# Kernel optimization log

Measured on AMD Instinct MI355X. Metric: run time of the kernel, lower is better.

The kernel has to match this reference:

```python
import jax, jax.numpy as jnp
import numpy as np
from jax.scipy.linalg import cholesky, solve_triangular, cho_solve

N, M, D = 16384, 2048, 8
VAR, LS = 1.0, 0.5      # RBF kernel hyperparameters (same for kernel_f and kernel_g)
JITTER = 1e-6
BATCH_RATE = 1.0
HALF_LOG_2PI = 0.5 * float(np.log(2.0 * np.pi))


def rbf(x1, x2):
    # K[i,j] = VAR * exp(-||x1_i - x2_j||^2 / (2 LS^2))
    d2 = (jnp.sum(x1 * x1, 1)[:, None] + jnp.sum(x2 * x2, 1)[None, :]
          - 2.0 * (x1 @ x2.T))
    return VAR * jnp.exp(-0.5 * d2 / (LS * LS))


def setup_inputs() -> dict:
    key = jax.random.key(0)
    ks = jax.random.split(key, 7)
    x = jax.random.normal(ks[0], (N, D), dtype=jnp.float32)
    y = jax.random.normal(ks[1], (N, 1), dtype=jnp.float32)
    z = 2.0 * jax.random.uniform(ks[2], (M, D), dtype=jnp.float32) - 1.0  # inducing inputs in [-1,1]^D
    q_m_f = 0.5 * jax.random.normal(ks[3], (M, 1), dtype=jnp.float32)
    q_m_g = 0.5 * jax.random.normal(ks[4], (M, 1), dtype=jnp.float32)
    # Cholesky-like params: identity plus small strictly-lower noise -> PD covariance
    q_L_f = jnp.eye(M, dtype=jnp.float32) + 0.01 * jnp.tril(
        jax.random.normal(ks[5], (M, M), dtype=jnp.float32), -1)
    q_L_g = jnp.eye(M, dtype=jnp.float32) + 0.01 * jnp.tril(
        jax.random.normal(ks[6], (M, M), dtype=jnp.float32), -1)
    return {"x": x, "y": y, "z": z, "q_m_f": q_m_f, "q_L_f": q_L_f,
            "q_m_g": q_m_g, "q_L_g": q_L_g}


def _gp_marginals_and_kl(x, z, q_m, q_L_raw):
    """Marginal posterior mean/var at x and KL(q(u)||p(u)) for one sparse GP."""
    L_S = jnp.tril(q_L_raw)                     # [M,M]
    Kuu = rbf(z, z) + JITTER * jnp.eye(M, dtype=x.dtype)
    Lk = cholesky(Kuu, lower=True)
    Kfu = rbf(x, z)                             # [N,M]
    # A = Kfu @ Kuu^{-1}
    A = cho_solve((Lk, True), Kfu.T).T          # [N,M]
    m = (A @ q_m)[:, 0]                         # [N]
    # diag(Kff + A (S - Kuu) A^T) = diag(Kff) + diag(A S A^T) - diag(Kfu A^T)
    S = L_S @ L_S.T
    diag_Kff = jnp.full((x.shape[0],), VAR, dtype=x.dtype)
    v = diag_Kff + jnp.sum((A @ S) * A, axis=1) - jnp.sum(A * Kfu, axis=1)
    # KL(N(q_m, S) || N(0, Kuu))
    alpha = solve_triangular(Lk, q_m, lower=True)       # Kuu^{-1/2} m
    W = solve_triangular(Lk, L_S, lower=True)           # Kuu^{-1/2} L_S
    logdet_K = 2.0 * jnp.sum(jnp.log(jnp.diag(Lk)))
    logdet_S = 2.0 * jnp.sum(jnp.log(jnp.abs(jnp.diag(L_S))))
    kl = 0.5 * (jnp.sum(W * W) + jnp.sum(alpha * alpha)
                - jnp.asarray(M, x.dtype) + logdet_K - logdet_S)
    return m, v, kl


def reference(x, y, z, q_m_f, q_L_f, q_m_g, q_L_g):
    m_f, v_f, kl_f = _gp_marginals_and_kl(x, z, q_m_f, q_L_f)
    m_g, v_g, kl_g = _gp_marginals_and_kl(x, z, q_m_g, q_L_g)
    yv = y[:, 0]
    # HetGaussian variational expectation (Saul et al. 2016):
    # E_q[log N(y | f, exp(g))] per point
    expectation = (-HALF_LOG_2PI - 0.5 * m_g
                   - 0.5 * ((yv - m_f) ** 2 + v_f) * jnp.exp(-m_g + 0.5 * v_g))
    elbo = BATCH_RATE * jnp.sum(expectation) - (kl_f + kl_g)
    return -elbo
```

## Files before the change

kernel.cpp:

```cpp
#include <hip/hip_runtime.h>
#include <math.h>

#define NN 16384
#define MM 2048
#define DD 8
#define NB 32
#define SZB ((size_t)16777216)

constexpr float HLOG2PI = 0.91893853320467274178f;

using short8  = __attribute__((ext_vector_type(8))) short;
using float4v = __attribute__((ext_vector_type(4))) float;

__device__ __forceinline__ float4v f4zero(){ float4v v; v[0]=0.f; v[1]=0.f; v[2]=0.f; v[3]=0.f; return v; }

__device__ __forceinline__ void bfsplit(float v, short& h, short& lo){
  unsigned b = __float_as_uint(v);
  h = (short)(b >> 16);
  float hf = __uint_as_float(b & 0xFFFF0000u);
  lo = (short)(__float_as_uint(v - hf) >> 16);
}
__device__ __forceinline__ float bf2f(short s){
  return __uint_as_float(((unsigned)(unsigned short)s) << 16);
}
__device__ __forceinline__ float4v mfma3(short8 ah, short8 al, short8 bh, short8 bl, float4v c){
  c = __builtin_amdgcn_mfma_f32_16x16x32_bf16(ah, bh, c, 0, 0, 0);
  c = __builtin_amdgcn_mfma_f32_16x16x32_bf16(ah, bl, c, 0, 0, 0);
  c = __builtin_amdgcn_mfma_f32_16x16x32_bf16(al, bh, c, 0, 0, 0);
  return c;
}

__device__ __forceinline__ float block_reduce(float v, float* scratch){
  int lane = threadIdx.x & 63;
  int w    = threadIdx.x >> 6;
  #pragma unroll
  for (int off=32; off; off>>=1) v += __shfl_down(v, off, 64);
  __syncthreads();
  if (lane==0) scratch[w] = v;
  __syncthreads();
  float r = 0.f;
  if (threadIdx.x < 4) r = scratch[threadIdx.x];
  if (w==0){ r += __shfl_down(r, 2, 64); r += __shfl_down(r, 1, 64); }
  return r;
}

__device__ __forceinline__ void stage64(float (*S)[68], const float* __restrict__ g, int ld, int t){
  #pragma unroll
  for (int p=t; p<1024; p+=256)
    *(float4*)&S[p>>4][(p&15)*4] = *(const float4*)&g[(size_t)(p>>4)*ld + (p&15)*4];
}
__device__ __forceinline__ void tile_gemm_step(float acc[4][4], const float (*As)[68], const float (*Bs)[68], int tx, int ty){
  for (int k=0;k<64;++k){
    float ar[4], bc4[4];
    #pragma unroll
    for (int u=0;u<4;++u){ ar[u]=As[ty*4+u][k]; bc4[u]=Bs[k][tx*4+u]; }
    #pragma unroll
    for (int u=0;u<4;++u)
      #pragma unroll
      for (int v=0;v<4;++v) acc[u][v] += ar[u]*bc4[v];
  }
}
__device__ __forceinline__ void tile_syrk_step(float acc[4][4], const float (*P)[68], const float (*Q)[68], int tx, int ty){
  for (int k=0;k<64;++k){
    float pr[4], qc[4];
    #pragma unroll
    for (int u=0;u<4;++u){ pr[u]=P[ty*4+u][k]; qc[u]=Q[tx*4+u][k]; }
    #pragma unroll
    for (int u=0;u<4;++u)
      #pragma unroll
      for (int v=0;v<4;++v) acc[u][v] += pr[u]*qc[v];
  }
}

__device__ __forceinline__ void factor64_reg(const float (*S)[68],
    float* __restrict__ lkd, float* __restrict__ sdg_, int d, int t){
  if (t < 64){
    float xr[64];
    #pragma unroll
    for (int c4=0;c4<16;++c4) *(float4*)&xr[c4*4] = *(const float4*)&S[t][c4*4];
    float myrp = 1.f;
    #pragma unroll
    for (int j=0;j<64;++j){
      float ajj = __shfl(xr[j], j, 64);
      float piv = sqrtf(fmaxf(ajj, 1e-20f));
      float rp  = 1.f/piv;
      float val = xr[j]*rp;
      if (t==j){ xr[j] = piv; myrp = rp; }
      else if (t>j) xr[j] = val;
      else val = 0.f;
      #pragma unroll
      for (int c=j+1;c<64;++c){
        float vc = __shfl(val, c, 64);
        if (c<=t) xr[c] -= val*vc;
      }
    }
    #pragma unroll
    for (int c=0;c<64;++c) if (c>t) xr[c] = 0.f;
    #pragma unroll
    for (int c4=0;c4<16;++c4)
      *(float4*)&lkd[d*4096 + t*64 + c4*4] = *(float4*)&xr[c4*4];
    sdg_[d*64 + t] = myrp;
  }
}


__global__ __launch_bounds__(256) void phase0_kernel(
    const float* __restrict__ z, float* __restrict__ kuu){
  __shared__ float As[64][68];
  __shared__ float Bs[64][68];
  const int t = threadIdx.x, tx = t & 15, ty = t >> 4;
  int idx = blockIdx.x;
  int r=0; while ((r+1)*(r+2)/2 <= idx) ++r;
  int c = idx - r*(r+1)/2;
  for (int p=t; p<128; p+=256){ int i=p>>1, h=p&1;
    *(float4*)&As[i][h*4] = *(const float4*)&z[(size_t)(r*64+i)*DD + h*4];
    *(float4*)&Bs[i][h*4] = *(const float4*)&z[(size_t)(c*64+i)*DD + h*4]; }
  __syncthreads();
  #pragma unroll
  for (int u=0;u<4;++u){
    float4 o;
    float* ov = (float*)&o;
    #pragma unroll
    for (int v=0;v<4;++v){
      float d2=0.f;
      #pragma unroll
      for (int d=0;d<8;++d){ float df=As[ty*4+u][d]-Bs[tx*4+v][d]; d2+=df*df; }
      float val = __expf(-2.f*d2);
      if (r*64+ty*4+u == c*64+tx*4+v) val += 1e-6f;
      ov[v] = val;
    }
    *(float4*)&kuu[(size_t)(r*64+ty*4+u)*MM + c*64 + tx*4] = o;
  }
}

__global__ __launch_bounds__(256) void diag0_kernel(
    const float* __restrict__ kuu, float* __restrict__ lkdiag, float* __restrict__ sdg){
  __shared__ float As[64][68];
  const int t = threadIdx.x;
  stage64(As, kuu, MM, t);
  __syncthreads();
  factor64_reg(As, lkdiag, sdg, 0, t);
}

__global__ __launch_bounds__(256) void panel_kernel(
    float* __restrict__ kuu, float* __restrict__ lkdiag,
    float* __restrict__ sdg, float* __restrict__ ltri, int kb){
  __shared__ float As[64][68];
  __shared__ float Bs[64][68];
  __shared__ float Cs[64][68];
  __shared__ float sd[64];
  const int t = threadIdx.x, tx = t & 15, ty = t >> 4;
  int idx = blockIdx.x;
  int r=0; while ((r+1)*(r+2)/2 <= idx) ++r;
  int c = idx - r*(r+1)/2;
  int bi = kb+1+r, bc = kb+1+c;
  stage64(Cs, lkdiag + kb*4096, 64, t);
  if (t < 64) sd[t] = sdg[kb*64 + t];
  stage64(As, kuu + (size_t)(bi*64)*MM + kb*64, MM, t);
  if (bc != bi) stage64(Bs, kuu + (size_t)(bc*64)*MM + kb*64, MM, t);
  __syncthreads();
  {
    int w = t>>6, l = t&63;
    if (w==0 || (w==1 && bc!=bi)){
      float (*S)[68] = (w==0)? As : Bs;
      float xr[64];
      #pragma unroll
      for (int c4=0;c4<16;++c4) *(float4*)&xr[c4*4] = *(const float4*)&S[l][c4*4];
      #pragma unroll
      for (int j=0;j<64;++j){
        float xj = xr[j]*sd[j];
        xr[j] = xj;
        #pragma unroll
        for (int cc=j+1;cc<64;++cc) xr[cc] -= xj*Cs[cc][j];
      }
      #pragma unroll
      for (int c4=0;c4<16;++c4) *(float4*)&S[l][c4*4] = *(float4*)&xr[c4*4];
    }
  }
  __syncthreads();
  if (bc == kb+1){
    for (int p=t;p<1024;p+=256)
      *(float4*)&ltri[(size_t)(bi*64+(p>>4))*MM + kb*64 + (p&15)*4] =
          *(float4*)&As[p>>4][(p&15)*4];
  }
  float acc[4][4] = {};
  tile_syrk_step(acc, As, (bc==bi)? As : Bs, tx, ty);
  if (bi==kb+1 && bc==kb+1){
    __syncthreads();
    #pragma unroll
    for (int u=0;u<4;++u)
      #pragma unroll
      for (int v=0;v<4;++v) Bs[ty*4+u][tx*4+v] = acc[u][v];
    __syncthreads();
    for (int p=t;p<1024;p+=256){
      int i=p>>4, c4=p&15;
      float4 kv = *(const float4*)&kuu[(size_t)(bi*64+i)*MM + bi*64 + c4*4];
      float4 bv = *(float4*)&Bs[i][c4*4];
      float4 o; o.x=kv.x-bv.x; o.y=kv.y-bv.y; o.z=kv.z-bv.z; o.w=kv.w-bv.w;
      *(float4*)&As[i][c4*4] = o;
    }
    __syncthreads();
    factor64_reg(As, lkdiag, sdg, kb+1, t);
  } else {
    #pragma unroll
    for (int u=0;u<4;++u){
      float4* dst = (float4*)&kuu[(size_t)(bi*64+ty*4+u)*MM + bc*64 + tx*4];
      float4 o = *dst;
      o.x-=acc[u][0]; o.y-=acc[u][1]; o.z-=acc[u][2]; o.w-=acc[u][3];
      *dst = o;
    }
  }
}

__global__ __launch_bounds__(256) void phase2_kernel(
    const float* __restrict__ lkdiag, float* __restrict__ linv){
  __shared__ float As[64][68];
  __shared__ float Bs[64][68];
  const int t = threadIdx.x, bid = blockIdx.x;
  stage64(As, lkdiag + bid*4096, 64, t);
  __syncthreads();
  if (t < 64){
    for (int j=0;j<64;++j){
      float s = (j==t)?1.f:0.f;
      for (int k=t;k<j;++k) s -= As[j][k]*Bs[k][t];
      Bs[j][t] = (j>=t)? s/As[j][j] : 0.f;
    }
  }
  __syncthreads();
  for (int p=t;p<1024;p+=256){ int i=p>>4, c4=p&15;
    *(float4*)&linv[(size_t)(bid*64+i)*MM + bid*64 + c4*4] = *(float4*)&Bs[i][c4*4]; }
}

__global__ __launch_bounds__(256) void p3l0_kernel(
    const float* __restrict__ ltri, float* __restrict__ linv){
  __shared__ float As[64][68];
  __shared__ float Bs[64][68];
  const int t = threadIdx.x, tx = t & 15, ty = t >> 4;
  int m = blockIdx.x;
  stage64(As, ltri + (size_t)((2*m+1)*64)*MM + (2*m)*64, MM, t);
  stage64(Bs, linv + (size_t)((2*m)*64)*MM   + (2*m)*64, MM, t);
  __syncthreads();
  float acc[4][4]={};
  tile_gemm_step(acc, As, Bs, tx, ty);
  __syncthreads();
  #pragma unroll
  for (int u=0;u<4;++u)
    #pragma unroll
    for (int v=0;v<4;++v) Bs[ty*4+u][tx*4+v] = acc[u][v];
  stage64(As, linv + (size_t)((2*m+1)*64)*MM + (2*m+1)*64, MM, t);
  __syncthreads();
  float o[4][4]={};
  tile_gemm_step(o, As, Bs, tx, ty);
  #pragma unroll
  for (int u=0;u<4;++u)
    *(float4*)&linv[(size_t)((2*m+1)*64+ty*4+u)*MM + (2*m)*64 + tx*4] =
        make_float4(-o[u][0],-o[u][1],-o[u][2],-o[u][3]);
}

__global__ __launch_bounds__(256) void p3l1_kernel(
    const float* __restrict__ ltri, float* __restrict__ linv, float* __restrict__ ptmp){
  __shared__ float As[64][68];
  __shared__ float Bs[64][68];
  const int t = threadIdx.x, tx = t & 15, ty = t >> 4;
  int m = blockIdx.x;
  float* pm = ptmp + (size_t)m*128*128;
  for (int ti=0; ti<2; ++ti)
    for (int tj=0; tj<2; ++tj){
      int rb = m*4 + 2 + ti, cb0 = m*4;
      float acc[4][4]={};
      for (int k=tj; k<2; ++k){
        __syncthreads();
        stage64(As, ltri + (size_t)(rb*64)*MM + (cb0+k)*64, MM, t);
        stage64(Bs, linv + (size_t)((cb0+k)*64)*MM + (cb0+tj)*64, MM, t);
        __syncthreads();
        tile_gemm_step(acc, As, Bs, tx, ty);
      }
      #pragma unroll
      for (int u=0;u<4;++u)
        *(float4*)&pm[(size_t)(ti*64+ty*4+u)*128 + tj*64 + tx*4] =
            make_float4(acc[u][0],acc[u][1],acc[u][2],acc[u][3]);
    }
  for (int ti=0; ti<2; ++ti)
    for (int tj=0; tj<2; ++tj){
      int rb = m*4 + 2 + ti;
      float acc[4][4]={};
      for (int k=0; k<=ti; ++k){
        __syncthreads();
        stage64(As, linv + (size_t)(rb*64)*MM + (m*4+2+k)*64, MM, t);
        stage64(Bs, pm + (size_t)(k*64)*128 + tj*64, 128, t);
        __syncthreads();
        tile_gemm_step(acc, As, Bs, tx, ty);
      }
      #pragma unroll
      for (int u=0;u<4;++u)
        *(float4*)&linv[(size_t)(rb*64+ty*4+u)*MM + (m*4+tj)*64 + tx*4] =
            make_float4(-acc[u][0],-acc[u][1],-acc[u][2],-acc[u][3]);
    }
}

__global__ __launch_bounds__(256) void p3lA_kernel(
    const float* __restrict__ ltri, const float* __restrict__ linv,
    float* __restrict__ ptmp, int s){
  __shared__ float As[64][68];
  __shared__ float Bs[64][68];
  const int t = threadIdx.x, tx = t & 15, ty = t >> 4;
  int nb = 1<<s, b = 64<<s;
  float* pmb = ptmp + (s==2 ? 131072 : (s==3 ? 393216 : 917504));
  int idx = blockIdx.x;
  int m = idx/(nb*nb), r2 = idx%(nb*nb);
  int ti = r2/nb, tj = r2%nb;
  int rb = m*2*nb + nb + ti, cb0 = m*2*nb;
  float acc[4][4]={};
  for (int k=tj; k<nb; ++k){
    __syncthreads();
    stage64(As, ltri + (size_t)(rb*64)*MM + (cb0+k)*64, MM, t);
    stage64(Bs, linv + (size_t)((cb0+k)*64)*MM + (cb0+tj)*64, MM, t);
    __syncthreads();
// ... 29 lines not shown
  #pragma unroll
  for (int u=0;u<4;++u)
    *(float4*)&linv[(size_t)(rb*64+ty*4+u)*MM + (m*2*nb+tj)*64 + tx*4] =
        make_float4(-acc[u][0],-acc[u][1],-acc[u][2],-acc[u][3]);
}

__global__ __launch_bounds__(256) void w_kernel(
    const float* __restrict__ linv, const float* __restrict__ qlf,
    const float* __restrict__ qlg, float* __restrict__ wf, float* __restrict__ wg){
  __shared__ float As[64][68];
  __shared__ float Bs[64][68];
  const int t = threadIdx.x, tx = t & 15, ty = t >> 4;
  int idx = blockIdx.x;
  int gp = idx/528, rem = idx%528;
  int bi=0; while ((bi+1)*(bi+2)/2 <= rem) ++bi;
  int bj = rem - bi*(bi+1)/2;
  const float* ql = gp ? qlg : qlf;
  float* w        = gp ? wg  : wf;
  float acc[4][4]={};
  for (int bk=bj; bk<=bi; ++bk){
    __syncthreads();
    stage64(As, linv + (size_t)(bi*64)*MM + bk*64, MM, t);
    stage64(Bs, ql   + (size_t)(bk*64)*MM + bj*64, MM, t);
    __syncthreads();
    if (bk==bj){
      for (int p=t;p<4096;p+=256){ int i=p>>6, c=p&63; if (i<c) Bs[i][c]=0.f; }
      __syncthreads();
    }
    tile_gemm_step(acc, As, Bs, tx, ty);
  }
  #pragma unroll
  for (int u=0;u<4;++u)
    *(float4*)&w[(size_t)(bi*64+ty*4+u)*MM + bj*64 + tx*4] =
        make_float4(acc[u][0],acc[u][1],acc[u][2],acc[u][3]);
}

__global__ __launch_bounds__(256) void alpha_kernel(
    const float* __restrict__ linv, const float* __restrict__ qmf,
    const float* __restrict__ qmg, float* __restrict__ af, float* __restrict__ ag){
  int t = threadIdx.x;
  int gw = blockIdx.x*4 + (t>>6), l = t&63;
  for (int job=gw; job<4096; job+=1024){
    int gp = job>>11, r = job&2047;
    const float* qm = gp ? qmg : qmf;
    float s=0.f;
    for (int c=l; c<=r; c+=64) s += linv[(size_t)r*MM+c]*qm[c];
    #pragma unroll
    for (int off=32; off; off>>=1) s += __shfl_down(s, off, 64);
    if (l==0) (gp ? ag : af)[r] = s;
  }
}


__global__ __launch_bounds__(256) void zfrag_kernel(const float* __restrict__ z,
    short* __restrict__ zfh, short* __restrict__ zfl, float* __restrict__ zn2){
  int zr = blockIdx.x*256 + threadIdx.x;
  float v[DD]; float s = 0.f;
  #pragma unroll
  for (int d=0; d<DD; ++d){ v[d] = z[zr*DD + d]; s += v[d]*v[d]; }
  zn2[zr] = s;
  size_t base = (size_t)(zr >> 4)*512 + (zr & 15)*32;
  #pragma unroll
  for (int k=0; k<32; ++k){
    short h = 0, lo = 0;
    if (k < DD) bfsplit(v[k], h, lo);
    zfh[base + k] = h; zfl[base + k] = lo;
  }
}

__global__ __launch_bounds__(256) void red_small(const float* __restrict__ lkd,
    const float* __restrict__ qlf, const float* __restrict__ qlg,
    const float* __restrict__ af, const float* __restrict__ ag,
    float* __restrict__ scal){
  __shared__ float scratch[4];
  float ldk=0, ldf=0, ldg=0, a2f=0, a2g=0;
  for (int i=threadIdx.x;i<MM;i+=256){
    int kb = i>>6, r = i&63;
    ldk += __logf(lkd[kb*4096 + r*64 + r]);
    ldf += __logf(fabsf(qlf[(size_t)i*MM+i]));
    ldg += __logf(fabsf(qlg[(size_t)i*MM+i]));
    float v = af[i]; a2f += v*v;
    v = ag[i];       a2g += v*v;
  }
  float r;
  r = block_reduce(ldk, scratch); if (threadIdx.x==0) scal[0] = 2.f*r;
  r = block_reduce(ldf, scratch); if (threadIdx.x==0) scal[1] = 2.f*r;
  r = block_reduce(ldg, scratch); if (threadIdx.x==0) scal[2] = 2.f*r;
  r = block_reduce(a2f, scratch); if (threadIdx.x==0) scal[3] = r;
  r = block_reduce(a2g, scratch); if (threadIdx.x==0) scal[4] = r;
}

__global__ __launch_bounds__(256) void redw_kernel(const float* __restrict__ wf,
    const float* __restrict__ wg, float* __restrict__ scal){
  __shared__ float scratch[4];
  size_t start  = (size_t)blockIdx.x*256 + threadIdx.x;
  size_t stride = (size_t)gridDim.x*256;
  float sf=0, sg=0;
  for (size_t p=start;p<(size_t)MM*MM;p+=stride){
    float v=wf[p]; sf += v*v;
    v=wg[p];       sg += v*v;
  }
  float r = block_reduce(sf, scratch);
  if (threadIdx.x==0) atomicAdd(&scal[5], r);
  r = block_reduce(sg, scratch);
  if (threadIdx.x==0) atomicAdd(&scal[6], r);
}

__global__ void kl_kernel(const float* __restrict__ scal, float* __restrict__ out){
  float klf = 0.5f*(scal[5] + scal[3] - (float)MM + scal[0] - scal[1]);
  float klg = 0.5f*(scal[6] + scal[4] - (float)MM + scal[0] - scal[2]);
  out[0] += klf + klg;
}

__global__ __launch_bounds__(256) void split_rowmajor(const float* __restrict__ src,
    short* __restrict__ dh, short* __restrict__ dl){
  int p = blockIdx.x*256 + threadIdx.x;
  int chunk = p >> 9, wi = p & 511;
  int mo = chunk >> 6, ko = chunk & 63;
  int row = mo*16 + (wi >> 5), col = ko*32 + (wi & 31);
  float v = src[(size_t)row*MM + col];
  short h, lo; bfsplit(v, h, lo);
  dh[p] = h; dl[p] = lo;
}

__global__ __launch_bounds__(256) void split_transpose(const float* __restrict__ src,
    short* __restrict__ dh, short* __restrict__ dl){
  __shared__ float tile[32][33];
  int t = threadIdx.x;
  int mb = blockIdx.x, kb = blockIdx.y;
  #pragma unroll
  for (int k=0;k<4;++k){
    int idx = t + k*256;
    int lr = idx >> 5, lc = idx & 31;
    tile[lr][lc] = src[(size_t)(kb*32+lr)*MM + mb*32 + lc];
  }
  __syncthreads();
  #pragma unroll
  for (int e=0;e<4;++e){
    int p = t*4 + e;
    int c = p >> 9, wi = p & 511;
    int i = (wi >> 5) & 15, kk = wi & 31;
    float v = tile[kk][c*16 + i];
    short h, lo; bfsplit(v, h, lo);
    size_t gp = ((size_t)(mb*2 + c)*64 + kb)*512 + wi;
    dh[gp] = h; dl[gp] = lo;
  }
}

__global__ __launch_bounds__(256, 2) void tt_mfma(
    const float* __restrict__ x, const float* __restrict__ zn2,
    const short* __restrict__ zfh, const short* __restrict__ zfl,
    const short* __restrict__ lvh, const short* __restrict__ lvl,
    short* __restrict__ tth, short* __restrict__ ttl){
  __shared__ __align__(16) short lAh[8192], lAl[8192], lBh[8192], lBl[8192];
  int t = threadIdx.x;
  int l = t & 63, w = t >> 6;
  int istrip = blockIdx.x, bj2 = blockIdx.y;
  int li = l & 15, q = l >> 4;
  int lofs = li*32 + q*8;
  int wn4 = (w>>1)*4, wm4 = (w&1)*4;

  short8 xh[2], xl[2];
  float xn2v[8];
  {
    float xn2t[2];
    #pragma unroll
    for (int tn=0; tn<2; ++tn){
      int n = istrip*128 + w*32 + tn*16 + li;
      const float4* xp = (const float4*)(x + (size_t)n*DD);
      float4 p0 = xp[0], p1 = xp[1];
      float v[8] = {p0.x,p0.y,p0.z,p0.w,p1.x,p1.y,p1.z,p1.w};
      float s = 0.f;
      #pragma unroll
      for (int d=0; d<8; ++d) s += v[d]*v[d];
      xn2t[tn] = s;
      short8 hh, ll;
      #pragma unroll
      for (int j=0; j<8; ++j){
        short h=0, lo=0;
        if (q==0) bfsplit(v[j], h, lo);
        hh[j]=h; ll[j]=lo;
      }
// ... 209 lines not shown
  int i = blockIdx.x*256 + threadIdx.x;
  float mf = lf[i], mg = lg[i];
  float vf = 1.f + vfq[i] - t2[i];
  float vg = 1.f + vgq[i] - t2[i];
  float dy = y[i] - mf;
  float e = -HLOG2PI - 0.5f*mg - 0.5f*(dy*dy + vf)*__expf(-mg + 0.5f*vg);
  float r = block_reduce(e, scratch);
  if (threadIdx.x==0) atomicAdd(out, -r);
}

extern "C" void kernel_launch(void* const* d_in, const int* in_sizes, int n_in,
                              void* d_out, int out_size, void* d_ws, size_t ws_size,
                              hipStream_t stream){
  (void)in_sizes; (void)n_in; (void)out_size; (void)ws_size;
  const float* x   = (const float*)d_in[0];
  const float* y   = (const float*)d_in[1];
  const float* z   = (const float*)d_in[2];
  const float* qmf = (const float*)d_in[3];
  const float* qlf = (const float*)d_in[4];
  const float* qmg = (const float*)d_in[5];
  const float* qlg = (const float*)d_in[6];
  float* out = (float*)d_out;
  char* Bw = (char*)d_ws;

  float* kuu  = (float*)Bw;
  float* linv = (float*)(Bw + SZB);
  float* wf   = (float*)(Bw + 2*SZB);
  float* wg   = (float*)(Bw + 3*SZB);
  short* lvh  = (short*)Bw;
  short* lvl  = (short*)(Bw + SZB/2);
  short* wfh  = (short*)(Bw + SZB);
  short* wfl  = (short*)(Bw + SZB + SZB/2);
  short* wgh  = (short*)(Bw + 2*SZB);
  short* wgl  = (short*)(Bw + 2*SZB + SZB/2);
  short* tth  = (short*)(Bw + 3*SZB);
  short* ttl  = (short*)(Bw + 3*SZB + (size_t)NN*MM*2);
  float* ltri   = (float*)(Bw + 4*SZB);
  float* ptmp   = (float*)(Bw + 5*SZB);
  float* lkdiag = (float*)(Bw + 5*SZB + (size_t)8388608);
  float* sdg    = (float*)(Bw + 5*SZB + (size_t)8388608 + (size_t)524288);
  float* sm   = (float*)(Bw + 3*SZB + (size_t)NN*MM*4);
  float* af = sm;          float* ag = af + MM;
  float* t2 = ag + MM;     float* lf = t2 + NN;   float* lg = lf + NN;
  float* vfq = lg + NN;    float* vgq = vfq + NN; float* scal = vgq + NN;
  float* zn2 = scal + 64 + 2048;
  short* zfh = (short*)(zn2 + MM);
  short* zfl = zfh + MM*32;

  hipMemsetAsync(out, 0, sizeof(float), stream);
  hipMemsetAsync(vfq, 0, (size_t)(2*NN + 64 + 2048)*sizeof(float), stream);
  hipMemsetAsync(wf,  0, 2*SZB, stream);
  hipMemsetAsync(linv,0, SZB,   stream);

  zfrag_kernel<<<MM/256, 256, 0, stream>>>(z, zfh, zfl, zn2);

  phase0_kernel<<<528, 256, 0, stream>>>(z, kuu);
  diag0_kernel<<<1, 256, 0, stream>>>(kuu, lkdiag, sdg);
  for (int kb = 0; kb < 31; ++kb){
    int T = NB - 1 - kb;
    panel_kernel<<<T*(T+1)/2, 256, 0, stream>>>(kuu, lkdiag, sdg, ltri, kb);
  }
  phase2_kernel<<<NB, 256, 0, stream>>>(lkdiag, linv);
  p3l0_kernel<<<16, 256, 0, stream>>>(ltri, linv);
  p3l1_kernel<<<8, 256, 0, stream>>>(ltri, linv, ptmp);
  for (int s = 2; s < 5; ++s){
    int nb = 1<<s, mc = 16>>s;
    p3lA_kernel<<<mc*nb*nb, 256, 0, stream>>>(ltri, linv, ptmp, s);
    p3lB_kernel<<<mc*nb*nb, 256, 0, stream>>>(linv, ptmp, s);
  }
  w_kernel<<<2*528, 256, 0, stream>>>(linv, qlf, qlg, wf, wg);
  alpha_kernel<<<256, 256, 0, stream>>>(linv, qmf, qmg, af, ag);

  red_small<<<1, 256, 0, stream>>>(lkdiag, qlf, qlg, af, ag, scal);
  redw_kernel<<<512, 256, 0, stream>>>(wf, wg, scal);
  kl_kernel<<<1, 1, 0, stream>>>(scal, out);

  split_rowmajor<<<MM*MM/256, 256, 0, stream>>>(linv, lvh, lvl);
  split_transpose<<<dim3(MM/32, MM/32), 256, 0, stream>>>(wf, wfh, wfl);
  split_transpose<<<dim3(MM/32, MM/32), 256, 0, stream>>>(wg, wgh, wgl);

  tt_mfma<<<dim3(NN/128, MM/128), 256, 0, stream>>>(x, zn2, zfh, zfl, lvh, lvl, tth, ttl);
  lin_v2<<<NN/4, 256, 0, stream>>>(tth, ttl, af, ag, t2, lf, lg);
  quad_mfma<<<dim3(NN/128, MM/128, 2), 256, 0, stream>>>(tth, ttl, wfh, wfl, wgh, wgl, vfq, vgq);
  final_kernel<<<NN/256, 256, 0, stream>>>(y, t2, lf, lg, vfq, vgq, out);
}
```

Measured before the change: 3.914 ms.

## Use 128-wide panels in blocked Cholesky to halve kernel launches

The right-looking blocked Cholesky now advances two 64-column blocks per step instead of one. Each launch solves the 128-wide panel and applies a rank-128 trailing update, and one block factors the next 128x128 diagonal. This cuts the serial panel launches from 31 to 15 and halves the number of read-modify-write passes over the trailing kuu tiles. In exchange the serial per-row triangular solves and diagonal factorization get longer, and shared memory per block rises to roughly 135KB, which may limit occupancy.

```diff
diff --git a/kernel.cpp b/kernel.cpp
--- a/kernel.cpp
+++ b/kernel.cpp
@@ -5,6 +5,7 @@
 #define MM 2048
 #define DD 8
 #define NB 32
+#define LDW 132
 #define SZB ((size_t)16777216)
 
 constexpr float HLOG2PI = 0.91893853320467274178f;
@@ -60,8 +61,14 @@
       for (int v=0;v<4;++v) acc[u][v] += ar[u]*bc4[v];
   }
 }
-__device__ __forceinline__ void tile_syrk_step(float acc[4][4], const float (*P)[68], const float (*Q)[68], int tx, int ty){
-  for (int k=0;k<64;++k){
+
+__device__ __forceinline__ void stage64h(float (*S)[LDW], int co, const float* __restrict__ g, int ld, int t){
+  #pragma unroll
+  for (int p=t; p<1024; p+=256)
+    *(float4*)&S[p>>4][co + (p&15)*4] = *(const float4*)&g[(size_t)(p>>4)*ld + (p&15)*4];
+}
+__device__ __forceinline__ void syrk132(float acc[4][4], const float (*P)[LDW], const float (*Q)[LDW], int ko, int tx, int ty){
+  for (int k=ko;k<ko+64;++k){
     float pr[4], qc[4];
     #pragma unroll
     for (int u=0;u<4;++u){ pr[u]=P[ty*4+u][k]; qc[u]=Q[tx*4+u][k]; }
@@ -71,13 +78,44 @@
       for (int v=0;v<4;++v) acc[u][v] += pr[u]*qc[v];
   }
 }
-
-__device__ __forceinline__ void factor64_reg(const float (*S)[68],
-    float* __restrict__ lkd, float* __restrict__ sdg_, int d, int t){
+__device__ __forceinline__ void trsm_row128(float* Srow, const float (*Cs)[LDW], const float* sd){
+  float a[64];
+  #pragma unroll
+  for (int c4=0;c4<16;++c4) *(float4*)&a[c4*4] = *(const float4*)&Srow[c4*4];
+  #pragma unroll
+  for (int j=0;j<64;++j){
+    float xj = a[j]*sd[j];
+    a[j] = xj;
+    #pragma unroll
+    for (int cc=j+1;cc<64;++cc) a[cc] -= xj*Cs[cc][j];
+  }
+  #pragma unroll
+  for (int c4=0;c4<16;++c4) *(float4*)&Srow[c4*4] = *(float4*)&a[c4*4];
+  float b[64];
+  #pragma unroll
+  for (int c4=0;c4<16;++c4) *(float4*)&b[c4*4] = *(const float4*)&Srow[64+c4*4];
+  for (int j=0;j<64;++j){
+    float xj = Srow[j];
+    #pragma unroll
+    for (int cc=0;cc<64;++cc) b[cc] -= xj*Cs[64+cc][j];
+  }
+  #pragma unroll
+  for (int j=0;j<64;++j){
+    float xj = b[j]*sd[64+j];
+    b[j] = xj;
+    #pragma unroll
+    for (int cc=j+1;cc<64;++cc) b[cc] -= xj*Cs[64+cc][64+j];
+  }
+  #pragma unroll
+  for (int c4=0;c4<16;++c4) *(float4*)&Srow[64+c4*4] = *(float4*)&b[c4*4];
+}
+
+__device__ __forceinline__ void factor64_p(float* S, float* __restrict__ lkd,
+    float* __restrict__ sdg_, float* sdl, int d, int t){
   if (t < 64){
     float xr[64];
     #pragma unroll
-    for (int c4=0;c4<16;++c4) *(float4*)&xr[c4*4] = *(const float4*)&S[t][c4*4];
+    for (int c4=0;c4<16;++c4) *(float4*)&xr[c4*4] = *(const float4*)&S[t*LDW + c4*4];
     float myrp = 1.f;
     #pragma unroll
     for (int j=0;j<64;++j){
@@ -97,10 +135,57 @@
     #pragma unroll
     for (int c=0;c<64;++c) if (c>t) xr[c] = 0.f;
     #pragma unroll
-    for (int c4=0;c4<16;++c4)
+    for (int c4=0;c4<16;++c4){
       *(float4*)&lkd[d*4096 + t*64 + c4*4] = *(float4*)&xr[c4*4];
+      *(float4*)&S[t*LDW + c4*4] = *(float4*)&xr[c4*4];
+    }
     sdg_[d*64 + t] = myrp;
-  }
+    sdl[t] = myrp;
+  }
+}
+
+__device__ void factor128(float (*Cs)[LDW], float* sd, float* __restrict__ lkd,
+    float* __restrict__ sdg_, float* __restrict__ ltri, int rs, int t){
+  factor64_p(&Cs[0][0], lkd, sdg_, sd, rs, t);
+  __syncthreads();
+  if (t < 64){
+    float xr[64];
+    #pragma unroll
+    for (int c4=0;c4<16;++c4) *(float4*)&xr[c4*4] = *(const float4*)&Cs[64+t][c4*4];
+    #pragma unroll
+    for (int j=0;j<64;++j){
+      float xj = xr[j]*sd[j];
+      xr[j] = xj;
+      #pragma unroll
+      for (int cc=j+1;cc<64;++cc) xr[cc] -= xj*Cs[cc][j];
+    }
+    #pragma unroll
+    for (int c4=0;c4<16;++c4) *(float4*)&Cs[64+t][c4*4] = *(float4*)&xr[c4*4];
+  }
+  __syncthreads();
+  {
+    const int tx = t & 15, ty = t >> 4;
+    for (int p=t;p<1024;p+=256)
+      *(float4*)&ltri[(size_t)((rs+1)*64+(p>>4))*MM + rs*64 + (p&15)*4] =
+          *(float4*)&Cs[64+(p>>4)][(p&15)*4];
+    float acc[4][4] = {};
+    for (int k=0;k<64;++k){
+      float pr[4], qc[4];
+      #pragma unroll
+      for (int u=0;u<4;++u){ pr[u]=Cs[64+ty*4+u][k]; qc[u]=Cs[64+tx*4+u][k]; }
+      #pragma unroll
+      for (int u=0;u<4;++u)
+        #pragma unroll
+        for (int v=0;v<4;++v) acc[u][v] += pr[u]*qc[v];
+    }
+    #pragma unroll
+    for (int u=0;u<4;++u)
+      #pragma unroll
+      for (int v=0;v<4;++v)
+        Cs[64+ty*4+u][64+tx*4+v] -= acc[u][v];
+  }
+  __syncthreads();
+  factor64_p(&Cs[64][64], lkd, sdg_, sd, rs+1, t);
 }
 
 
@@ -133,75 +218,86 @@
   }
 }
 
-__global__ __launch_bounds__(256) void diag0_kernel(
-    const float* __restrict__ kuu, float* __restrict__ lkdiag, float* __restrict__ sdg){
-  __shared__ float As[64][68];
+__global__ __launch_bounds__(256) void diag128_0_kernel(
+    const float* __restrict__ kuu, float* __restrict__ lkdiag,
+    float* __restrict__ sdg, float* __restrict__ ltri){
+  __shared__ float Cs[128][LDW];
+  __shared__ float sd[128];
   const int t = threadIdx.x;
-  stage64(As, kuu, MM, t);
-  __syncthreads();
-  factor64_reg(As, lkdiag, sdg, 0, t);
-}
-
-__global__ __launch_bounds__(256) void panel_kernel(
+  for (int p=t;p<1024;p+=256){
+    int r=p>>4, c0=(p&15)*4;
+    *(float4*)&Cs[r][c0]       = *(const float4*)&kuu[(size_t)r*MM + c0];
+    *(float4*)&Cs[64+r][c0]    = *(const float4*)&kuu[(size_t)(64+r)*MM + c0];
+    *(float4*)&Cs[64+r][64+c0] = *(const float4*)&kuu[(size_t)(64+r)*MM + 64 + c0];
+  }
+  __syncthreads();
+  factor128(Cs, sd, lkdiag, sdg, ltri, 0, t);
+}
+
+__global__ __launch_bounds__(256) void panel128_kernel(
     float* __restrict__ kuu, float* __restrict__ lkdiag,
     float* __restrict__ sdg, float* __restrict__ ltri, int kb){
-  __shared__ float As[64][68];
-  __shared__ float Bs[64][68];
-  __shared__ float Cs[64][68];
-  __shared__ float sd[64];
+  __shared__ float As[64][LDW];
+  __shared__ float Bs[64][LDW];
+  __shared__ float Cs[128][LDW];
+  __shared__ float sd[128];
   const int t = threadIdx.x, tx = t & 15, ty = t >> 4;
-  int idx = blockIdx.x;
-  int r=0; while ((r+1)*(r+2)/2 <= idx) ++r;
-  int c = idx - r*(r+1)/2;
-  int bi = kb+1+r, bc = kb+1+c;
-  stage64(Cs, lkdiag + kb*4096, 64, t);
-  if (t < 64) sd[t] = sdg[kb*64 + t];
-  stage64(As, kuu + (size_t)(bi*64)*MM + kb*64, MM, t);
-  if (bc != bi) stage64(Bs, kuu + (size_t)(bc*64)*MM + kb*64, MM, t);
+  const int d0 = 2*kb, d1 = 2*kb+1, rs = 2*kb+2;
+  for (int p=t;p<1024;p+=256){
+    int r=p>>4, c0=(p&15)*4;
+    *(float4*)&Cs[r][c0]       = *(const float4*)&lkdiag[d0*4096 + r*64 + c0];
+    *(float4*)&Cs[64+r][c0]    = *(const float4*)&ltri[(size_t)(d1*64+r)*MM + d0*64 + c0];
+    *(float4*)&Cs[64+r][64+c0] = *(const float4*)&lkdiag[d1*4096 + r*64 + c0];
+  }
+  if (t < 128) sd[t] = sdg[d0*64 + t];
+  const int bid = blockIdx.x;
+  const bool isdiag = (bid == 0);
+  int bi = rs, bc = rs;
+  if (!isdiag){
+    int idx = bid + 2;
+    int r=0; while ((r+1)*(r+2)/2 <= idx) ++r;
+    int c = idx - r*(r+1)/2;
+    bi = rs + r; bc = rs + c;
+    stage64h(As, 0,  kuu + (size_t)(bi*64)*MM + d0*64, MM, t);
+    stage64h(As, 64, kuu + (size_t)(bi*64)*MM + d1*64, MM, t);
+    if (bc != bi){
+      stage64h(Bs, 0,  kuu + (size_t)(bc*64)*MM + d0*64, MM, t);
+      stage64h(Bs, 64, kuu + (size_t)(bc*64)*MM + d1*64, MM, t);
+    }
+  } else {
+    stage64h(As, 0,  kuu + (size_t)(rs*64)*MM + d0*64, MM, t);
+    stage64h(As, 64, kuu + (size_t)(rs*64)*MM + d1*64, MM, t);
+    stage64h(Bs, 0,  kuu + (size_t)((rs+1)*64)*MM + d0*64, MM, t);
+    stage64h(Bs, 64, kuu + (size_t)((rs+1)*64)*MM + d1*64, MM, t);
+  }
   __syncthreads();
   {
     int w = t>>6, l = t&63;
-    if (w==0 || (w==1 && bc!=bi)){
-      float (*S)[68] = (w==0)? As : Bs;
-      float xr[64];
-      #pragma unroll
-      for (int c4=0;c4<16;++c4) *(float4*)&xr[c4*4] = *(const float4*)&S[l][c4*4];
-      #pragma unroll
-      for (int j=0;j<64;++j){
-        float xj = xr[j]*sd[j];
-        xr[j] = xj;
-        #pragma unroll
-        for (int cc=j+1;cc<64;++cc) xr[cc] -= xj*Cs[cc][j];
-      }
-      #pragma unroll
-      for (int c4=0;c4<16;++c4) *(float4*)&S[l][c4*4] = *(float4*)&xr[c4*4];
-    }
-  }
-  __syncthreads();
-  if (bc == kb+1){
-    for (int p=t;p<1024;p+=256)
-      *(float4*)&ltri[(size_t)(bi*64+(p>>4))*MM + kb*64 + (p&15)*4] =
-          *(float4*)&As[p>>4][(p&15)*4];
-  }
-  float acc[4][4] = {};
-  tile_syrk_step(acc, As, (bc==bi)? As : Bs, tx, ty);
-  if (bi==kb+1 && bc==kb+1){
-    __syncthreads();
-    #pragma unroll
-    for (int u=0;u<4;++u)
-      #pragma unroll
-      for (int v=0;v<4;++v) Bs[ty*4+u][tx*4+v] = acc[u][v];
-    __syncthreads();
+    bool doB = isdiag || (bc != bi);
+    if (w==0) trsm_row128(&As[l][0], (const float (*)[LDW])Cs, sd);
+    else if (w==1 && doB) trsm_row128(&Bs[l][0], (const float (*)[LDW])Cs, sd);
+  }
+  __syncthreads();
+  if (isdiag){
     for (int p=t;p<1024;p+=256){
-      int i=p>>4, c4=p&15;
-      float4 kv = *(const float4*)&kuu[(size_t)(bi*64+i)*MM + bi*64 + c4*4];
-      float4 bv = *(float4*)&Bs[i][c4*4];
-      float4 o; o.x=kv.x-bv.x; o.y=kv.y-bv.y; o.z=kv.z-bv.z; o.w=kv.w-bv.w;
-      *(float4*)&As[i][c4*4] = o;
-    }
-    __syncthreads();
-    factor64_reg(As, lkdiag, sdg, kb+1, t);
-  } else {
+      int r=p>>4, c0=(p&15)*4;
+      *(float4*)&ltri[(size_t)(rs*64+r)*MM + d0*64 + c0]     = *(float4*)&As[r][c0];
+      *(float4*)&ltri[(size_t)(rs*64+r)*MM + d1*64 + c0]     = *(float4*)&As[r][64+c0];
+      *(float4*)&ltri[(size_t)((rs+1)*64+r)*MM + d0*64 + c0] = *(float4*)&Bs[r][c0];
+      *(float4*)&ltri[(size_t)((rs+1)*64+r)*MM + d1*64 + c0] = *(float4*)&Bs[r][64+c0];
+    }
+  } else if (bc == rs){
+    for (int p=t;p<1024;p+=256){
+      int r=p>>4, c0=(p&15)*4;
+      *(float4*)&ltri[(size_t)(bi*64+r)*MM + d0*64 + c0] = *(float4*)&As[r][c0];
+      *(float4*)&ltri[(size_t)(bi*64+r)*MM + d1*64 + c0] = *(float4*)&As[r][64+c0];
+    }
+  }
+  if (!isdiag){
+    float acc[4][4] = {};
+    const float (*Q)[LDW] = (bc==bi)? (const float (*)[LDW])As : (const float (*)[LDW])Bs;
+    syrk132(acc, (const float (*)[LDW])As, Q, 0,  tx, ty);
+    syrk132(acc, (const float (*)[LDW])As, Q, 64, tx, ty);
     #pragma unroll
     for (int u=0;u<4;++u){
       float4* dst = (float4*)&kuu[(size_t)(bi*64+ty*4+u)*MM + bc*64 + tx*4];
@@ -209,6 +305,35 @@
       o.x-=acc[u][0]; o.y-=acc[u][1]; o.z-=acc[u][2]; o.w-=acc[u][3];
       *dst = o;
     }
+  } else {
+    float a11[4][4]={}, a21[4][4]={}, a22[4][4]={};
+    syrk132(a11, (const float (*)[LDW])As, (const float (*)[LDW])As, 0,  tx, ty);
+    syrk132(a11, (const float (*)[LDW])As, (const float (*)[LDW])As, 64, tx, ty);
+    syrk132(a21, (const float (*)[LDW])Bs, (const float (*)[LDW])As, 0,  tx, ty);
+    syrk132(a21, (const float (*)[LDW])Bs, (const float (*)[LDW])As, 64, tx, ty);
+    syrk132(a22, (const float (*)[LDW])Bs, (const float (*)[LDW])Bs, 0,  tx, ty);
+    syrk132(a22, (const float (*)[LDW])Bs, (const float (*)[LDW])Bs, 64, tx, ty);
+    __syncthreads();
+    #pragma unroll
+    for (int u=0;u<4;++u){
+      float4 k11 = *(const float4*)&kuu[(size_t)(rs*64+ty*4+u)*MM + rs*64 + tx*4];
+      Cs[ty*4+u][tx*4  ] = k11.x - a11[u][0];
+      Cs[ty*4+u][tx*4+1] = k11.y - a11[u][1];
+      Cs[ty*4+u][tx*4+2] = k11.z - a11[u][2];
+      Cs[ty*4+u][tx*4+3] = k11.w - a11[u][3];
+      float4 k21 = *(const float4*)&kuu[(size_t)((rs+1)*64+ty*4+u)*MM + rs*64 + tx*4];
+      Cs[64+ty*4+u][tx*4  ] = k21.x - a21[u][0];
+      Cs[64+ty*4+u][tx*4+1] = k21.y - a21[u][1];
+      Cs[64+ty*4+u][tx*4+2] = k21.z - a21[u][2];
+      Cs[64+ty*4+u][tx*4+3] = k21.w - a21[u][3];
+      float4 k22 = *(const float4*)&kuu[(size_t)((rs+1)*64+ty*4+u)*MM + (rs+1)*64 + tx*4];
+      Cs[64+ty*4+u][64+tx*4  ] = k22.x - a22[u][0];
+      Cs[64+ty*4+u][64+tx*4+1] = k22.y - a22[u][1];
+      Cs[64+ty*4+u][64+tx*4+2] = k22.z - a22[u][2];
+      Cs[64+ty*4+u][64+tx*4+3] = k22.w - a22[u][3];
+    }
+    __syncthreads();
+    factor128(Cs, sd, lkdiag, sdg, ltri, rs, t);
   }
 }
 
@@ -792,10 +917,11 @@
   zfrag_kernel<<<MM/256, 256, 0, stream>>>(z, zfh, zfl, zn2);
 
   phase0_kernel<<<528, 256, 0, stream>>>(z, kuu);
-  diag0_kernel<<<1, 256, 0, stream>>>(kuu, lkdiag, sdg);
-  for (int kb = 0; kb < 31; ++kb){
-    int T = NB - 1 - kb;
-    panel_kernel<<<T*(T+1)/2, 256, 0, stream>>>(kuu, lkdiag, sdg, ltri, kb);
+  diag128_0_kernel<<<1, 256, 0, stream>>>(kuu, lkdiag, sdg, ltri);
+  for (int kb = 0; kb < 15; ++kb){
+    int T = 30 - 2*kb;
+    int ntiles = T*(T+1)/2;
+    panel128_kernel<<<ntiles - 2, 256, 0, stream>>>(kuu, lkdiag, sdg, ltri, kb);
   }
   phase2_kernel<<<NB, 256, 0, stream>>>(lkdiag, linv);
   p3l0_kernel<<<16, 256, 0, stream>>>(ltri, linv);
```

Result: slower. 4.903 ms (+25.3%).

## Merge small kernels to cut launch count in Cholesky and inverse setup

Applied to the files above, without the earlier changes.

Folds the z-fragment prep and the first diagonal factorization into the Kuu build kernel. The last four Cholesky panel steps move into a single-block tail kernel, and the diagonal-block inversion joins the first two inverse levels in one kernel. The three split kernels become one launch. This removes many tiny launches and their gaps. In exchange, the tail steps and the diagonal inversion now run serially in one block or a few blocks, which lowers parallelism in those stages.

```diff
diff --git a/kernel.cpp b/kernel.cpp
--- a/kernel.cpp
+++ b/kernel.cpp
@@ -103,23 +103,74 @@
   }
 }
 
+__device__ __forceinline__ void factor64_t(const float (*S)[68], float (*D)[68],
+    float* sdl, float* __restrict__ lkd, float* __restrict__ sdg_, int d, int t){
+  if (t < 64){
+    float xr[64];
+    #pragma unroll
+    for (int c4=0;c4<16;++c4) *(float4*)&xr[c4*4] = *(const float4*)&S[t][c4*4];
+    float myrp = 1.f;
+    #pragma unroll
+    for (int j=0;j<64;++j){
+      float ajj = __shfl(xr[j], j, 64);
+      float piv = sqrtf(fmaxf(ajj, 1e-20f));
+      float rp  = 1.f/piv;
+      float val = xr[j]*rp;
+      if (t==j){ xr[j] = piv; myrp = rp; }
+      else if (t>j) xr[j] = val;
+      else val = 0.f;
+      #pragma unroll
+      for (int c=j+1;c<64;++c){
+        float vc = __shfl(val, c, 64);
+        if (c<=t) xr[c] -= val*vc;
+      }
+    }
+    #pragma unroll
+    for (int c=0;c<64;++c) if (c>t) xr[c] = 0.f;
+    #pragma unroll
+    for (int c4=0;c4<16;++c4){
+      *(float4*)&lkd[d*4096 + t*64 + c4*4] = *(float4*)&xr[c4*4];
+      *(float4*)&D[t][c4*4] = *(float4*)&xr[c4*4];
+    }
+    sdg_[d*64 + t] = myrp;
+    sdl[t] = myrp;
+  }
+}
+
 
 __global__ __launch_bounds__(256) void phase0_kernel(
-    const float* __restrict__ z, float* __restrict__ kuu){
+    const float* __restrict__ z, float* __restrict__ kuu,
+    short* __restrict__ zfh, short* __restrict__ zfl, float* __restrict__ zn2,
+    float* __restrict__ lkdiag, float* __restrict__ sdg){
   __shared__ float As[64][68];
   __shared__ float Bs[64][68];
   const int t = threadIdx.x, tx = t & 15, ty = t >> 4;
-  int idx = blockIdx.x;
+  const int bid = blockIdx.x;
+  if (bid >= 528){
+    int zr = (bid-528)*256 + t;
+    float v[DD]; float s = 0.f;
+    #pragma unroll
+    for (int d=0; d<DD; ++d){ v[d] = z[zr*DD + d]; s += v[d]*v[d]; }
+    zn2[zr] = s;
+    size_t base = (size_t)(zr >> 4)*512 + (zr & 15)*32;
+    #pragma unroll
+    for (int k=0; k<32; ++k){
+      short h = 0, lo = 0;
+      if (k < DD) bfsplit(v[k], h, lo);
+      zfh[base + k] = h; zfl[base + k] = lo;
+    }
+    return;
+  }
+  int idx = bid;
   int r=0; while ((r+1)*(r+2)/2 <= idx) ++r;
   int c = idx - r*(r+1)/2;
   for (int p=t; p<128; p+=256){ int i=p>>1, h=p&1;
     *(float4*)&As[i][h*4] = *(const float4*)&z[(size_t)(r*64+i)*DD + h*4];
     *(float4*)&Bs[i][h*4] = *(const float4*)&z[(size_t)(c*64+i)*DD + h*4]; }
   __syncthreads();
-  #pragma unroll
-  for (int u=0;u<4;++u){
-    float4 o;
-    float* ov = (float*)&o;
+  float kv[4][4];
+  #pragma unroll
+  for (int u=0;u<4;++u)
     #pragma unroll
     for (int v=0;v<4;++v){
       float d2=0.f;
@@ -127,19 +178,21 @@
       for (int d=0;d<8;++d){ float df=As[ty*4+u][d]-Bs[tx*4+v][d]; d2+=df*df; }
       float val = __expf(-2.f*d2);
       if (r*64+ty*4+u == c*64+tx*4+v) val += 1e-6f;
-      ov[v] = val;
-    }
-    *(float4*)&kuu[(size_t)(r*64+ty*4+u)*MM + c*64 + tx*4] = o;
-  }
-}
-
-__global__ __launch_bounds__(256) void diag0_kernel(
-    const float* __restrict__ kuu, float* __restrict__ lkdiag, float* __restrict__ sdg){
-  __shared__ float As[64][68];
-  const int t = threadIdx.x;
-  stage64(As, kuu, MM, t);
-  __syncthreads();
-  factor64_reg(As, lkdiag, sdg, 0, t);
+      kv[u][v] = val;
+    }
+  #pragma unroll
+  for (int u=0;u<4;++u)
+    *(float4*)&kuu[(size_t)(r*64+ty*4+u)*MM + c*64 + tx*4] =
+        make_float4(kv[u][0],kv[u][1],kv[u][2],kv[u][3]);
+  if (idx == 0){
+    __syncthreads();
+    #pragma unroll
+    for (int u=0;u<4;++u)
+      #pragma unroll
+      for (int v=0;v<4;++v) As[ty*4+u][tx*4+v] = kv[u][v];
+    __syncthreads();
+    factor64_reg(As, lkdiag, sdg, 0, t);
+  }
 }
 
 __global__ __launch_bounds__(256) void panel_kernel(
@@ -212,57 +265,130 @@
   }
 }
 
-__global__ __launch_bounds__(256) void phase2_kernel(
-    const float* __restrict__ lkdiag, float* __restrict__ linv){
+__global__ __launch_bounds__(256) void tail_kernel(
+    float* __restrict__ kuu, float* __restrict__ lkdiag,
+    float* __restrict__ sdg, float* __restrict__ ltri){
   __shared__ float As[64][68];
   __shared__ float Bs[64][68];
-  const int t = threadIdx.x, bid = blockIdx.x;
-  stage64(As, lkdiag + bid*4096, 64, t);
-  __syncthreads();
-  if (t < 64){
-    for (int j=0;j<64;++j){
-      float s = (j==t)?1.f:0.f;
-      for (int k=t;k<j;++k) s -= As[j][k]*Bs[k][t];
-      Bs[j][t] = (j>=t)? s/As[j][j] : 0.f;
-    }
-  }
-  __syncthreads();
-  for (int p=t;p<1024;p+=256){ int i=p>>4, c4=p&15;
-    *(float4*)&linv[(size_t)(bid*64+i)*MM + bid*64 + c4*4] = *(float4*)&Bs[i][c4*4]; }
-}
-
-__global__ __launch_bounds__(256) void p3l0_kernel(
-    const float* __restrict__ ltri, float* __restrict__ linv){
+  __shared__ float Cs[64][68];
+  __shared__ float Ds[64][68];
+  __shared__ float sd[64], sd2[64];
+  const int t = threadIdx.x, tx = t & 15, ty = t >> 4;
+  stage64(Cs, lkdiag + 27*4096, 64, t);
+  if (t < 64) sd[t] = sdg[27*64 + t];
+  for (int kb=27; kb<31; ++kb){
+    int T = 31-kb, ntiles = T*(T+1)/2;
+    for (int idx=0; idx<ntiles; ++idx){
+      int r=0; while ((r+1)*(r+2)/2 <= idx) ++r;
+      int c = idx - r*(r+1)/2;
+      int bi = kb+1+r, bc = kb+1+c;
+      __syncthreads();
+      stage64(As, kuu + (size_t)(bi*64)*MM + kb*64, MM, t);
+      if (bc != bi) stage64(Bs, kuu + (size_t)(bc*64)*MM + kb*64, MM, t);
+      __syncthreads();
+      {
+        int w = t>>6, l = t&63;
+        if (w==0 || (w==1 && bc!=bi)){
+          float (*S)[68] = (w==0)? As : Bs;
+          float xr[64];
+          #pragma unroll
+          for (int c4=0;c4<16;++c4) *(float4*)&xr[c4*4] = *(const float4*)&S[l][c4*4];
+          #pragma unroll
+          for (int j=0;j<64;++j){
+            float xj = xr[j]*sd[j];
+            xr[j] = xj;
+            #pragma unroll
+            for (int cc=j+1;cc<64;++cc) xr[cc] -= xj*Cs[cc][j];
+          }
+          #pragma unroll
+          for (int c4=0;c4<16;++c4) *(float4*)&S[l][c4*4] = *(float4*)&xr[c4*4];
+        }
+      }
+      __syncthreads();
+      if (bc == kb+1){
+        for (int p=t;p<1024;p+=256)
+          *(float4*)&ltri[(size_t)(bi*64+(p>>4))*MM + kb*64 + (p&15)*4] =
+              *(float4*)&As[p>>4][(p&15)*4];
+      }
+      float acc[4][4] = {};
+      tile_syrk_step(acc, As, (bc==bi)? As : Bs, tx, ty);
+      if (bi==kb+1 && bc==kb+1){
+        __syncthreads();
+        #pragma unroll
+        for (int u=0;u<4;++u)
+          #pragma unroll
+          for (int v=0;v<4;++v) Bs[ty*4+u][tx*4+v] = acc[u][v];
+        __syncthreads();
+        for (int p=t;p<1024;p+=256){
+          int i=p>>4, c4=p&15;
+          float4 kv = *(const float4*)&kuu[(size_t)(bi*64+i)*MM + bi*64 + c4*4];
+          float4 bv = *(float4*)&Bs[i][c4*4];
+          float4 o; o.x=kv.x-bv.x; o.y=kv.y-bv.y; o.z=kv.z-bv.z; o.w=kv.w-bv.w;
+          *(float4*)&As[i][c4*4] = o;
+        }
+        __syncthreads();
+        factor64_t(As, Ds, sd2, lkdiag, sdg, kb+1, t);
+      } else {
+        #pragma unroll
+        for (int u=0;u<4;++u){
+          float4* dst = (float4*)&kuu[(size_t)(bi*64+ty*4+u)*MM + bc*64 + tx*4];
+          float4 o = *dst;
+          o.x-=acc[u][0]; o.y-=acc[u][1]; o.z-=acc[u][2]; o.w-=acc[u][3];
+          *dst = o;
+        }
+      }
+    }
+    __syncthreads();
+    for (int p=t;p<1024;p+=256)
+      *(float4*)&Cs[p>>4][(p&15)*4] = *(const float4*)&Ds[p>>4][(p&15)*4];
+    if (t < 64) sd[t] = sd2[t];
+  }
+}
+
+__global__ __launch_bounds__(256) void p3head_kernel(
+    const float* __restrict__ lkdiag, const float* __restrict__ ltri,
+    float* __restrict__ linv, float* __restrict__ ptmp){
   __shared__ float As[64][68];
   __shared__ float Bs[64][68];
   const int t = threadIdx.x, tx = t & 15, ty = t >> 4;
-  int m = blockIdx.x;
-  stage64(As, ltri + (size_t)((2*m+1)*64)*MM + (2*m)*64, MM, t);
-  stage64(Bs, linv + (size_t)((2*m)*64)*MM   + (2*m)*64, MM, t);
-  __syncthreads();
-  float acc[4][4]={};
-  tile_gemm_step(acc, As, Bs, tx, ty);
-  __syncthreads();
-  #pragma unroll
-  for (int u=0;u<4;++u)
-    #pragma unroll
-    for (int v=0;v<4;++v) Bs[ty*4+u][tx*4+v] = acc[u][v];
-  stage64(As, linv + (size_t)((2*m+1)*64)*MM + (2*m+1)*64, MM, t);
-  __syncthreads();
-  float o[4][4]={};
-  tile_gemm_step(o, As, Bs, tx, ty);
-  #pragma unroll
-  for (int u=0;u<4;++u)
-    *(float4*)&linv[(size_t)((2*m+1)*64+ty*4+u)*MM + (2*m)*64 + tx*4] =
-        make_float4(-o[u][0],-o[u][1],-o[u][2],-o[u][3]);
-}
-
-__global__ __launch_bounds__(256) void p3l1_kernel(
-    const float* __restrict__ ltri, float* __restrict__ linv, float* __restrict__ ptmp){
-  __shared__ float As[64][68];
-  __shared__ float Bs[64][68];
-  const int t = threadIdx.x, tx = t & 15, ty = t >> 4;
-  int m = blockIdx.x;
+  const int m = blockIdx.x;
+  for (int d=4*m; d<4*m+4; ++d){
+    __syncthreads();
+    stage64(As, lkdiag + d*4096, 64, t);
+    __syncthreads();
+    if (t < 64){
+      for (int j=0;j<64;++j){
+        float s = (j==t)?1.f:0.f;
+        for (int k=t;k<j;++k) s -= As[j][k]*Bs[k][t];
+        Bs[j][t] = (j>=t)? s/As[j][j] : 0.f;
+      }
+    }
+    __syncthreads();
+    for (int p=t;p<1024;p+=256){ int i=p>>4, c4=p&15;
+      *(float4*)&linv[(size_t)(d*64+i)*MM + d*64 + c4*4] = *(float4*)&Bs[i][c4*4]; }
+  }
+  for (int q2=0;q2<2;++q2){
+    int mm = 2*m + q2;
+    __syncthreads();
+    stage64(As, ltri + (size_t)((2*mm+1)*64)*MM + (2*mm)*64, MM, t);
+    stage64(Bs, linv + (size_t)((2*mm)*64)*MM   + (2*mm)*64, MM, t);
+    __syncthreads();
+    float acc[4][4]={};
+    tile_gemm_step(acc, As, Bs, tx, ty);
+    __syncthreads();
+    #pragma unroll
+    for (int u=0;u<4;++u)
+      #pragma unroll
+      for (int v=0;v<4;++v) Bs[ty*4+u][tx*4+v] = acc[u][v];
+    stage64(As, linv + (size_t)((2*mm+1)*64)*MM + (2*mm+1)*64, MM, t);
+    __syncthreads();
+    float o[4][4]={};
+    tile_gemm_step(o, As, Bs, tx, ty);
+    #pragma unroll
+    for (int u=0;u<4;++u)
+      *(float4*)&linv[(size_t)((2*mm+1)*64+ty*4+u)*MM + (2*mm)*64 + tx*4] =
+          make_float4(-o[u][0],-o[u][1],-o[u][2],-o[u][3]);
+  }
   float* pm = ptmp + (size_t)m*128*128;
   for (int ti=0; ti<2; ++ti)
     for (int tj=0; tj<2; ++tj){
@@ -398,22 +524,6 @@
 }
 
 
-__global__ __launch_bounds__(256) void zfrag_kernel(const float* __restrict__ z,
-    short* __restrict__ zfh, short* __restrict__ zfl, float* __restrict__ zn2){
-  int zr = blockIdx.x*256 + threadIdx.x;
-  float v[DD]; float s = 0.f;
-  #pragma unroll
-  for (int d=0; d<DD; ++d){ v[d] = z[zr*DD + d]; s += v[d]*v[d]; }
-  zn2[zr] = s;
-  size_t base = (size_t)(zr >> 4)*512 + (zr & 15)*32;
-  #pragma unroll
-  for (int k=0; k<32; ++k){
-    short h = 0, lo = 0;
-    if (k < DD) bfsplit(v[k], h, lo);
-    zfh[base + k] = h; zfl[base + k] = lo;
-  }
-}
-
 __global__ __launch_bounds__(256) void red_small(const float* __restrict__ lkd,
     const float* __restrict__ qlf, const float* __restrict__ qlg,
     const float* __restrict__ af, const float* __restrict__ ag,
@@ -458,22 +568,31 @@
   out[0] += klf + klg;
 }
 
-__global__ __launch_bounds__(256) void split_rowmajor(const float* __restrict__ src,
-    short* __restrict__ dh, short* __restrict__ dl){
-  int p = blockIdx.x*256 + threadIdx.x;
-  int chunk = p >> 9, wi = p & 511;
-  int mo = chunk >> 6, ko = chunk & 63;
-  int row = mo*16 + (wi >> 5), col = ko*32 + (wi & 31);
-  float v = src[(size_t)row*MM + col];
-  short h, lo; bfsplit(v, h, lo);
-  dh[p] = h; dl[p] = lo;
-}
-
-__global__ __launch_bounds__(256) void split_transpose(const float* __restrict__ src,
-    short* __restrict__ dh, short* __restrict__ dl){
+__global__ __launch_bounds__(256) void split_all(
+    const float* __restrict__ linv, const float* __restrict__ wf,
+    const float* __restrict__ wg, short* __restrict__ lvh, short* __restrict__ lvl,
+    short* __restrict__ wfh, short* __restrict__ wfl,
+    short* __restrict__ wgh, short* __restrict__ wgl){
   __shared__ float tile[32][33];
-  int t = threadIdx.x;
-  int mb = blockIdx.x, kb = blockIdx.y;
+  const int t = threadIdx.x;
+  const int bid = blockIdx.x;
+  if (bid < 16384){
+    int p = bid*256 + t;
+    int chunk = p >> 9, wi = p & 511;
+    int mo = chunk >> 6, ko = chunk & 63;
+    int row = mo*16 + (wi >> 5), col = ko*32 + (wi & 31);
+    float v = linv[(size_t)row*MM + col];
+    short h, lo; bfsplit(v, h, lo);
+    lvh[p] = h; lvl[p] = lo;
+    return;
+  }
+  int idx2 = bid - 16384;
+  int zz = idx2 >> 12;
+  int rem = idx2 & 4095;
+  int mb = rem & 63, kb = rem >> 6;
+  const float* src = zz ? wg : wf;
+  short* dh = zz ? wgh : wfh;
+  short* dl = zz ? wgl : wfl;
   #pragma unroll
   for (int k=0;k<4;++k){
     int idx = t + k*256;
@@ -789,17 +908,13 @@
   hipMemsetAsync(wf,  0, 2*SZB, stream);
   hipMemsetAsync(linv,0, SZB,   stream);
 
-  zfrag_kernel<<<MM/256, 256, 0, stream>>>(z, zfh, zfl, zn2);
-
-  phase0_kernel<<<528, 256, 0, stream>>>(z, kuu);
-  diag0_kernel<<<1, 256, 0, stream>>>(kuu, lkdiag, sdg);
-  for (int kb = 0; kb < 31; ++kb){
+  phase0_kernel<<<536, 256, 0, stream>>>(z, kuu, zfh, zfl, zn2, lkdiag, sdg);
+  for (int kb = 0; kb < 27; ++kb){
     int T = NB - 1 - kb;
     panel_kernel<<<T*(T+1)/2, 256, 0, stream>>>(kuu, lkdiag, sdg, ltri, kb);
   }
-  phase2_kernel<<<NB, 256, 0, stream>>>(lkdiag, linv);
-  p3l0_kernel<<<16, 256, 0, stream>>>(ltri, linv);
-  p3l1_kernel<<<8, 256, 0, stream>>>(ltri, linv, ptmp);
+  tail_kernel<<<1, 256, 0, stream>>>(kuu, lkdiag, sdg, ltri);
+  p3head_kernel<<<8, 256, 0, stream>>>(lkdiag, ltri, linv, ptmp);
   for (int s = 2; s < 5; ++s){
     int nb = 1<<s, mc = 16>>s;
     p3lA_kernel<<<mc*nb*nb, 256, 0, stream>>>(ltri, linv, ptmp, s);
@@ -812,9 +927,7 @@
   redw_kernel<<<512, 256, 0, stream>>>(wf, wg, scal);
   kl_kernel<<<1, 1, 0, stream>>>(scal, out);
 
-  split_rowmajor<<<MM*MM/256, 256, 0, stream>>>(linv, lvh, lvl);
-  split_transpose<<<dim3(MM/32, MM/32), 256, 0, stream>>>(wf, wfh, wfl);
-  split_transpose<<<dim3(MM/32, MM/32), 256, 0, stream>>>(wg, wgh, wgl);
+  split_all<<<24576, 256, 0, stream>>>(linv, wf, wg, lvh, lvl, wfh, wfl, wgh, wgl);
 
   tt_mfma<<<dim3(NN/128, MM/128), 256, 0, stream>>>(x, zn2, zfh, zfl, lvh, lvl, tth, ttl);
   lin_v2<<<NN/4, 256, 0, stream>>>(tth, ttl, af, ag, t2, lf, lg);
```

After: 4.359 ms. 1.11x slower.
